# Kernel tuning notes

Measured on AMD Instinct MI355X. Metric: run time of the kernel, lower is better.

## Reference

```python
import jax, jax.numpy as jnp
import numpy as np

B, C, H, W = 8, 256, 64, 64
CR = C // 8  # reduced channels for query/key


def setup_inputs() -> dict:
    key = jax.random.key(0)
    ks = jax.random.split(key, 10)
    s = 0.02
    return {
        "x": jax.random.normal(ks[0], (B, C, H, W), dtype=jnp.float32),
        "cross_modal_features": jax.random.normal(ks[1], (B, C, H, W), dtype=jnp.float32),
        "wq": jax.random.normal(ks[2], (CR, C), dtype=jnp.float32) * s,
        "bq": jnp.zeros((CR,), dtype=jnp.float32),
        "wk": jax.random.normal(ks[3], (CR, C), dtype=jnp.float32) * s,
        "bk": jnp.zeros((CR,), dtype=jnp.float32),
        "wv": jax.random.normal(ks[4], (C, C), dtype=jnp.float32) * s,
        "bv": jnp.zeros((C,), dtype=jnp.float32),
        "wo": jax.random.normal(ks[5], (C, C), dtype=jnp.float32) * s,
        "bo": jnp.zeros((C,), dtype=jnp.float32),
        "gamma": jnp.zeros((1,), dtype=jnp.float32),
    }


def _conv1x1(w, b, t):
    # t: (B, Cin, HW) -> (B, Cout, HW); 1x1 conv == channel matmul
    return jnp.einsum("oc,bcn->bon", w, t) + b[None, :, None]


def reference(x, cross_modal_features, wq, bq, wk, bk, wv, bv, wo, bo, gamma):
    b, c, h, w = x.shape
    n = h * w
    xf = x.reshape(b, c, n)
    ff = cross_modal_features.reshape(b, c, n)
    q = _conv1x1(wq, bq, xf)          # (B, CR, N)
    k = _conv1x1(wk, bk, ff)          # (B, CR, N)
    v = _conv1x1(wv, bv, ff)          # (B, C, N)
    # attention[b,i,j] = softmax_j(q[b,:,i] . k[b,:,j])
    scores = jnp.einsum("bdi,bdj->bij", q, k)
    attn = jax.nn.softmax(scores, axis=-1)
    # out[b,c,i] = sum_j v[b,c,j] * attn[b,i,j]
    out = jnp.einsum("bcj,bij->bci", v, attn)
    out = _conv1x1(wo, bo, out).reshape(b, c, h, w)
    return gamma[0] * out + x
```

## Files before the change

### kernel.cpp

```cpp
#include <hip/hip_runtime.h>
#include <hip/hip_bf16.h>
#include <math.h>

#define B_  8
#define C_  256
#define CR_ 32
#define N_  4096

typedef __attribute__((ext_vector_type(8)))  short bf16x8;
typedef __attribute__((ext_vector_type(16))) float f32x16;
typedef __attribute__((ext_vector_type(4)))  int   int4v;

__device__ inline unsigned short f2b(float x) {
    __hip_bfloat16 h = __float2bfloat16(x);
    return __builtin_bit_cast(unsigned short, h);
}

#define GLL16(gsrc, ldst) \
    __builtin_amdgcn_global_load_lds((const __attribute__((address_space(1))) void*)(gsrc), \
                                     (__attribute__((address_space(3))) void*)(ldst), 16, 0, 0)

__global__ void pack_kernel(
    const float* __restrict__ wq, const float* __restrict__ bq,
    const float* __restrict__ wk, const float* __restrict__ bk,
    const float* __restrict__ wv, const float* __restrict__ bv,
    const float* __restrict__ wo,
    unsigned short* __restrict__ W1, unsigned short* __restrict__ W2,
    float* __restrict__ Bs1)
{
    const int r = blockIdx.x, t = threadIdx.x;
    const float L2E = 1.44269504088896340736f;
    if (r < 320) {
        float w;
        if (r < 32)      w = wq[r * C_ + t] * L2E;
        else if (r < 64) w = wk[(r - 32) * C_ + t];
        else             w = wv[(r - 64) * C_ + t];
        W1[r * C_ + t] = f2b(w);
        if (t == 0)
            Bs1[r] = (r < 32) ? bq[r] * L2E : ((r < 64) ? bk[r - 32] : bv[r - 64]);
    } else {
        W2[(r - 320) * C_ + t] = f2b(wo[(r - 320) * C_ + t]);
    }
}

__global__ __launch_bounds__(256) void convT_kernel(
    const float* __restrict__ x, const float* __restrict__ f,
    unsigned short* __restrict__ xT, unsigned short* __restrict__ fT)
{
    __shared__ float tile[64][65];
    const int t  = threadIdx.x;
    const int n0 = blockIdx.x * 64;
    const int c0 = blockIdx.y * 64;
    const int z  = blockIdx.z;
    const int b  = z >> 1;
    const float* src = (z & 1) ? f : x;
    unsigned short* dst = (z & 1) ? fT : xT;
    const size_t so = (size_t)b * C_ * N_;

    #pragma unroll
    for (int it = 0; it < 4; ++it) {
        const int cl = it * 16 + (t >> 4);
        *(float4*)&tile[cl][(t & 15) * 4] =
            *(const float4*)&src[so + (size_t)(c0 + cl) * N_ + n0 + (t & 15) * 4];
    }
    __syncthreads();

    const int nl = t >> 2;
    const int cg = (t & 3) * 16;
    unsigned short* drow = dst + ((size_t)b * N_ + n0 + nl) * C_ + c0 + cg;
    int4v w0, w1;
    #pragma unroll
    for (int e = 0; e < 4; ++e)
        w0[e] = (int)(((unsigned)f2b(tile[cg + 2*e][nl])) |
                      (((unsigned)f2b(tile[cg + 2*e + 1][nl])) << 16));
    #pragma unroll
    for (int e = 0; e < 4; ++e)
        w1[e] = (int)(((unsigned)f2b(tile[cg + 8 + 2*e][nl])) |
                      (((unsigned)f2b(tile[cg + 9 + 2*e][nl])) << 16));
    *(int4v*)(drow)     = w0;
    *(int4v*)(drow + 8) = w1;
}

__device__ __forceinline__ void gemm_mainloop(
    const unsigned short* __restrict__ Asrc,
    const unsigned short* __restrict__ Bsrc,
    unsigned short (*Ab)[32 * 32], unsigned short (*Bb)[256 * 32],
    int w, int l, f32x16& acc0, f32x16& acc1)
{
    const int jl = l & 31, hi = l >> 5;
    const int fj = (jl >> 1) & 3;

#define STAGE(KK, BUF) { \
    _Pragma("unroll") \
    for (int p = 0; p < 4; ++p) { \
        const int idx = p * 256 + w * 64 + l; \
        const int row = idx >> 2, slot = idx & 3; \
        GLL16(Bsrc + (size_t)row * 256 + (KK) * 32 + (slot ^ ((row >> 1) & 3)) * 8, \
              Bb[BUF] + (size_t)(p * 256 + w * 64) * 8); \
    } \
    if (w == 0) { \
        _Pragma("unroll") \
        for (int qq = 0; qq < 2; ++qq) { \
            const int idx = qq * 64 + l; \
            const int row = idx >> 2, slot = idx & 3; \
            GLL16(Asrc + (size_t)row * 256 + (KK) * 32 + (slot ^ ((row >> 1) & 3)) * 8, \
                  Ab[BUF] + (size_t)(qq * 64) * 8); \
        } \
    } }

    STAGE(0, 0)
    __syncthreads();

    for (int kk = 0; kk < 8; ++kk) {
        const int cur = kk & 1;
        if (kk < 7) STAGE(kk + 1, cur ^ 1)

        const unsigned short* Ac = Ab[cur];
        const unsigned short* Bc = Bb[cur];
        const bf16x8 af0 = *(const bf16x8*)&Ac[jl * 32 + ((hi ^ fj) * 8)];
        const bf16x8 af1 = *(const bf16x8*)&Ac[jl * 32 + (((2 + hi) ^ fj) * 8)];
        const int r0 = w * 64 + jl, r1 = w * 64 + 32 + jl;
        const bf16x8 bf00 = *(const bf16x8*)&Bc[r0 * 32 + ((hi ^ fj) * 8)];
        const bf16x8 bf01 = *(const bf16x8*)&Bc[r0 * 32 + (((2 + hi) ^ fj) * 8)];
        const bf16x8 bf10 = *(const bf16x8*)&Bc[r1 * 32 + ((hi ^ fj) * 8)];
        const bf16x8 bf11 = *(const bf16x8*)&Bc[r1 * 32 + (((2 + hi) ^ fj) * 8)];

        acc0 = __builtin_amdgcn_mfma_f32_32x32x16_bf16(af0, bf00, acc0, 0, 0, 0);
        acc0 = __builtin_amdgcn_mfma_f32_32x32x16_bf16(af1, bf01, acc0, 0, 0, 0);
        acc1 = __builtin_amdgcn_mfma_f32_32x32x16_bf16(af0, bf10, acc1, 0, 0, 0);
        acc1 = __builtin_amdgcn_mfma_f32_32x32x16_bf16(af1, bf11, acc1, 0, 0, 0);
        __syncthreads();
    }
#undef STAGE
}

__global__ __launch_bounds__(256) void qkv_gemm(
    const unsigned short* __restrict__ xT, const unsigned short* __restrict__ fT,
    const unsigned short* __restrict__ W1, const float* __restrict__ Bs1,
    unsigned short* __restrict__ qT, unsigned short* __restrict__ kT,
    unsigned short* __restrict__ v)
{
    __shared__ __align__(16) unsigned short Ab[2][32 * 32];
    __shared__ __align__(16) unsigned short Bb[2][256 * 32];

    const int t = threadIdx.x;
    const int w = t >> 6, l = t & 63;
    const int jl = l & 31, hi = l >> 5;
    const int bid = blockIdx.x;
    const int b  = bid & 7;
    const int r_ = bid >> 3;
    const int mt = r_ % 10;
    const int nt = r_ / 10;

    const unsigned short* Asrc = W1 + (size_t)mt * 32 * C_;
    const unsigned short* Bsrc = ((mt == 0) ? xT : fT) + (size_t)b * N_ * C_
                               + (size_t)nt * 256 * C_;

    f32x16 acc0 = (f32x16)0.f, acc1 = (f32x16)0.f;
    gemm_mainloop(Asrc, Bsrc, Ab, Bb, w, l, acc0, acc1);

    const int m0 = mt * 32;
    const int nb = nt * 256 + w * 64;
    if (mt <= 1) {
        unsigned short* dst = ((mt == 0) ? qT : kT) + (size_t)b * N_ * CR_;
        #pragma unroll
        for (int ns = 0; ns < 2; ++ns) {
            const f32x16& A = ns ? acc1 : acc0;
            const int n = nb + ns * 32 + jl;
            #pragma unroll
            for (int r4 = 0; r4 < 4; ++r4) {
                const float4 bi = *(const float4*)&Bs1[m0 + r4 * 8 + 4 * hi];
                const unsigned int d0 = (unsigned)f2b(A[r4*4+0] + bi.x) |
                                        ((unsigned)f2b(A[r4*4+1] + bi.y) << 16);
                const unsigned int d1 = (unsigned)f2b(A[r4*4+2] + bi.z) |
                                        ((unsigned)f2b(A[r4*4+3] + bi.w) << 16);
                *(uint2*)(dst + (size_t)n * CR_ + r4 * 8 + 4 * hi) = make_uint2(d0, d1);
            }
        }
    } else {
        unsigned short* dst = v + (size_t)b * C_ * N_;
        #pragma unroll
        for (int ns = 0; ns < 2; ++ns) {
            const f32x16& A = ns ? acc1 : acc0;
            const int n = nb + ns * 32 + jl;
            #pragma unroll
            for (int r4 = 0; r4 < 4; ++r4) {
                const float4 bi = *(const float4*)&Bs1[m0 + r4 * 8 + 4 * hi];
                #pragma unroll
                for (int e = 0; e < 4; ++e) {
                    const int c = m0 - 64 + e + 8 * r4 + 4 * hi;
                    dst[(size_t)c * N_ + n] = f2b(A[r4*4+e] + ((const float*)&bi)[e]);
                }
            }
        }
    }
}

__device__ inline void softmax_tile(const f32x16& s, float& lsum,
                                    bf16x8& pf0, bf16x8& pf1)
{
    float ps = 0.f;
    int wd[8];
    #pragma unroll
    for (int r = 0; r < 16; r += 2) {
        float e0 = __builtin_amdgcn_exp2f(s[r]);
        float e1 = __builtin_amdgcn_exp2f(s[r + 1]);
        ps += e0 + e1;
        int pk;
        asm("v_cvt_pk_bf16_f32 %0, %1, %2" : "=v"(pk) : "v"(e0), "v"(e1));
        wd[r >> 1] = pk;
    }
    lsum += ps;
    asm volatile("v_permlane32_swap_b32 %0, %1" : "+v"(wd[0]), "+v"(wd[2]));
    asm volatile("v_permlane32_swap_b32 %0, %1" : "+v"(wd[1]), "+v"(wd[3]));
    asm volatile("v_permlane32_swap_b32 %0, %1" : "+v"(wd[4]), "+v"(wd[6]));
    asm volatile("v_permlane32_swap_b32 %0, %1" : "+v"(wd[5]), "+v"(wd[7]));
    union { int4v i4; bf16x8 h8; } u0, u1;
    u0.i4 = (int4v){ wd[0], wd[1], wd[2], wd[3] };
    u1.i4 = (int4v){ wd[4], wd[5], wd[6], wd[7] };
    pf0 = u0.h8; pf1 = u1.h8;
}

__global__ __launch_bounds__(512) void attn_kernel(
    const unsigned short* __restrict__ qT, const unsigned short* __restrict__ kT,
    const unsigned short* __restrict__ v, unsigned short* __restrict__ aoT)
{
    __shared__ __align__(16) unsigned short Vt[2][256 * 64];
    __shared__ float lsx[2][512];

    const int t  = threadIdx.x;
    const int w  = t >> 6;
    const int l  = t & 63;
    const int jl = l & 31;
    const int hi = l >> 5;
    const int js = w & 1;
    const int ig = (w >> 1) & 1;
    const int cs = w >> 2;

    const int bid = blockIdx.x;
    const int b   = bid & 7;
    const int it  = bid >> 3;
    const int i0  = it * 128 + ig * 64;

    const unsigned short* qTb = qT + (size_t)b * N_ * CR_;
    const unsigned short* kTb = kT + (size_t)b * N_ * CR_;
    const unsigned short* vb  = v  + (size_t)b * C_ * N_;

    const bf16x8 q00 = *(const bf16x8*)(qTb + (size_t)(i0 + jl) * CR_ + hi * 8);
    const bf16x8 q01 = *(const bf16x8*)(qTb + (size_t)(i0 + jl) * CR_ + 16 + hi * 8);
    const bf16x8 q10 = *(const bf16x8*)(qTb + (size_t)(i0 + 32 + jl) * CR_ + hi * 8);
    const bf16x8 q11 = *(const bf16x8*)(qTb + (size_t)(i0 + 32 + jl) * CR_ + 16 + hi * 8);

    const unsigned short* kln = kTb + (size_t)(js * 32 + jl) * CR_ + hi * 8;

    const unsigned short* vsrc[4];
    int vdst[4];
    #pragma unroll
    for (int p = 0; p < 4; ++p) {
        const int idx = p * 512 + t;
        const int row = idx >> 3, slot = idx & 7;
        vsrc[p] = vb + (size_t)row * N_ + (slot ^ (row & 7)) * 8;
        vdst[p] = idx * 8;
    }

    f32x16 a00 = (f32x16)0.f, a01 = (f32x16)0.f, a02 = (f32x16)0.f, a03 = (f32x16)0.f;
    f32x16 a10 = (f32x16)0.f, a11 = (f32x16)0.f, a12 = (f32x16)0.f, a13 = (f32x16)0.f;
    float ls0 = 0.f, ls1 = 0.f;

    #pragma unroll
    for (int p = 0; p < 4; ++p) GLL16(vsrc[p], &Vt[0][vdst[p]]);
    bf16x8 kc0 = *(const bf16x8*)(kln);
    bf16x8 kc1 = *(const bf16x8*)(kln + 16);
    __syncthreads();

    int voff0[4], voff1[4];
    #pragma unroll
    for (int ct = 0; ct < 4; ++ct) {
        const int rv = cs * 128 + ct * 32 + jl;
        voff0[ct] = rv * 64 + (((js * 4 + hi)     ^ (rv & 7)) * 8);
        voff1[ct] = rv * 64 + (((js * 4 + 2 + hi) ^ (rv & 7)) * 8);
    }

    for (int jt = 0; jt < N_ / 64; ++jt) {
        const int cur = jt & 1;
        bf16x8 kn0 = kc0, kn1 = kc1;
        if (jt + 1 < N_ / 64) {
            const size_t jn = (size_t)(jt + 1) * 64;
            #pragma unroll
            for (int p = 0; p < 4; ++p) GLL16(vsrc[p] + jn, &Vt[cur ^ 1][vdst[p]]);
            kn0 = *(const bf16x8*)(kln + jn * CR_);
            kn1 = *(const bf16x8*)(kln + jn * CR_ + 16);
        }

        __builtin_amdgcn_s_setprio(1);
        f32x16 s0 = (f32x16)0.f, s1 = (f32x16)0.f;
        s0 = __builtin_amdgcn_mfma_f32_32x32x16_bf16(kc0, q00, s0, 0, 0, 0);
        s0 = __builtin_amdgcn_mfma_f32_32x32x16_bf16(kc1, q01, s0, 0, 0, 0);
        s1 = __builtin_amdgcn_mfma_f32_32x32x16_bf16(kc0, q10, s1, 0, 0, 0);
        s1 = __builtin_amdgcn_mfma_f32_32x32x16_bf16(kc1, q11, s1, 0, 0, 0);
        __builtin_amdgcn_s_setprio(0);

        bf16x8 p00, p01, p10, p11;
        softmax_tile(s0, ls0, p00, p01);
        softmax_tile(s1, ls1, p10, p11);

        __builtin_amdgcn_s_setprio(1);
#define PVSTEP(CT, AA, AB) { \
        const bf16x8 v0_ = *(const bf16x8*)&Vt[cur][voff0[CT]]; \
        const bf16x8 v1_ = *(const bf16x8*)&Vt[cur][voff1[CT]]; \
        AA = __builtin_amdgcn_mfma_f32_32x32x16_bf16(v0_, p00, AA, 0, 0, 0); \
        AA = __builtin_amdgcn_mfma_f32_32x32x16_bf16(v1_, p01, AA, 0, 0, 0); \
        AB = __builtin_amdgcn_mfma_f32_32x32x16_bf16(v0_, p10, AB, 0, 0, 0); \
        AB = __builtin_amdgcn_mfma_f32_32x32x16_bf16(v1_, p11, AB, 0, 0, 0); }
        PVSTEP(0, a00, a10)
        PVSTEP(1, a01, a11)
        PVSTEP(2, a02, a12)
        PVSTEP(3, a03, a13)
#undef PVSTEP
        __builtin_amdgcn_s_setprio(0);

        __syncthreads();
        kc0 = kn0; kc1 = kn1;
    }

    ls0 += __shfl_xor(ls0, 32);
    ls1 += __shfl_xor(ls1, 32);

    lsx[0][w * 64 + l] = ls0;
    lsx[1][w * 64 + l] = ls1;
    float* As = (float*)&Vt[0][0];
    const int base = (w >> 1) * 4096;

#define STORE_ACC(A, CT) { _Pragma("unroll") \
    for (int r = 0; r < 16; ++r) As[base + (CT) * 1024 + r * 64 + l] = A[r]; }
#define ADD_ACC(A, CT) { _Pragma("unroll") \
    for (int r = 0; r < 16; ++r) A[r] += As[base + (CT) * 1024 + r * 64 + l]; }

    __syncthreads();
    if (js == 1) { STORE_ACC(a00, 0) STORE_ACC(a01, 1) STORE_ACC(a02, 2) STORE_ACC(a03, 3) }
    __syncthreads();
    if (js == 0) { ADD_ACC(a00, 0) ADD_ACC(a01, 1) ADD_ACC(a02, 2) ADD_ACC(a03, 3) }
    __syncthreads();
    if (js == 1) { STORE_ACC(a10, 0) STORE_ACC(a11, 1) STORE_ACC(a12, 2) STORE_ACC(a13, 3) }
    __syncthreads();
    if (js == 0) {
        ADD_ACC(a10, 0) ADD_ACC(a11, 1) ADD_ACC(a12, 2) ADD_ACC(a13, 3)

        const float ra = 1.f / (ls0 + lsx[0][(w + 1) * 64 + l]);
        const float rb = 1.f / (ls1 + lsx[1][(w + 1) * 64 + l]);
        unsigned short* aoTb = aoT + (size_t)b * N_ * C_;
        const int ica = i0 + jl, icb = i0 + 32 + jl;
#define EPI(ACC, CT, COL, RL) { _Pragma("unroll") \
    for (int r4 = 0; r4 < 4; ++r4) { \
        const unsigned int d0 = (unsigned)f2b(ACC[r4*4+0] * (RL)) | \
                                ((unsigned)f2b(ACC[r4*4+1] * (RL)) << 16); \
        const unsigned int d1 = (unsigned)f2b(ACC[r4*4+2] * (RL)) | \
                                ((unsigned)f2b(ACC[r4*4+3] * (RL)) << 16); \
        *(uint2*)(aoTb + (size_t)(COL) * C_ + cs * 128 + (CT) * 32 + r4 * 8 + 4 * hi) \
            = make_uint2(d0, d1); } }
        EPI(a00, 0, ica, ra)
        EPI(a01, 1, ica, ra)
        EPI(a02, 2, ica, ra)
        EPI(a03, 3, ica, ra)
        EPI(a10, 0, icb, rb)
        EPI(a11, 1, icb, rb)
        EPI(a12, 2, icb, rb)
        EPI(a13, 3, icb, rb)
#undef EPI
    }
#undef STORE_ACC
#undef ADD_ACC
}

__global__ __launch_bounds__(256) void out_gemm(
    const unsigned short* __restrict__ aoT, const unsigned short* __restrict__ W2,
    const float* __restrict__ bo, const float* __restrict__ gamma,
    const float* __restrict__ x, float* __restrict__ out)
{
    __shared__ __align__(16) unsigned short Ab[2][32 * 32];
    __shared__ __align__(16) unsigned short Bb[2][256 * 32];

    const int t = threadIdx.x;
    const int w = t >> 6, l = t & 63;
    const int jl = l & 31, hi = l >> 5;
    const int bid = blockIdx.x;
    const int b  = bid & 7;
    const int r_ = bid >> 3;
    const int mt = r_ & 7;
    const int nt = r_ >> 3;

    const unsigned short* Asrc = W2 + (size_t)mt * 32 * C_;
    const unsigned short* Bsrc = aoT + (size_t)b * N_ * C_ + (size_t)nt * 256 * C_;

    f32x16 acc0 = (f32x16)0.f, acc1 = (f32x16)0.f;
    gemm_mainloop(Asrc, Bsrc, Ab, Bb, w, l, acc0, acc1);

    const float gm = gamma[0];
    const int m0 = mt * 32;
    const int nb = nt * 256 + w * 64;
    #pragma unroll
    for (int ns = 0; ns < 2; ++ns) {
        const f32x16& A = ns ? acc1 : acc0;
        const int n = nb + ns * 32 + jl;
        #pragma unroll
        for (int r4 = 0; r4 < 4; ++r4) {
            const float4 bi = *(const float4*)&bo[m0 + r4 * 8 + 4 * hi];
            #pragma unroll
            for (int e = 0; e < 4; ++e) {
                const int c = m0 + e + 8 * r4 + 4 * hi;
                const size_t o = ((size_t)b * C_ + c) * N_ + n;
                out[o] = fmaf(gm, A[r4*4+e] + ((const float*)&bi)[e], x[o]);
            }
        }
    }
}

extern "C" void kernel_launch(void* const* d_in, const int* in_sizes, int n_in,
                              void* d_out, int out_size, void* d_ws, size_t ws_size,
                              hipStream_t stream)
{
    const float* x     = (const float*)d_in[0];
    const float* f     = (const float*)d_in[1];
    const float* wq    = (const float*)d_in[2];
    const float* bq    = (const float*)d_in[3];
    const float* wk    = (const float*)d_in[4];
    const float* bk    = (const float*)d_in[5];
    const float* wv    = (const float*)d_in[6];
    const float* bv    = (const float*)d_in[7];
    const float* wo    = (const float*)d_in[8];
    const float* bo    = (const float*)d_in[9];
    const float* gamma = (const float*)d_in[10];
    float* out = (float*)d_out;

    float* Bs1 = (float*)d_ws;
    unsigned short* W1 = (unsigned short*)(Bs1 + 320);
    unsigned short* W2 = W1 + 320 * C_;
    unsigned short* xT = W2 + 256 * C_;
    unsigned short* fT = xT + (size_t)B_ * N_ * C_;
    unsigned short* qT = fT + (size_t)B_ * N_ * C_;
    unsigned short* kT = qT + (size_t)B_ * N_ * CR_;
    unsigned short* vv = kT + (size_t)B_ * N_ * CR_;
    unsigned short* aoT = vv + (size_t)B_ * C_ * N_;

    pack_kernel<<<dim3(576), 256, 0, stream>>>(wq, bq, wk, bk, wv, bv, wo, W1, W2, Bs1);
    convT_kernel<<<dim3(64, 4, 16), 256, 0, stream>>>(x, f, xT, fT);
    qkv_gemm<<<dim3(1280), 256, 0, stream>>>(xT, fT, W1, Bs1, qT, kT, vv);
    attn_kernel<<<dim3(256), 512, 0, stream>>>(qT, kT, vv, aoT);
    out_gemm<<<dim3(1024), 256, 0, stream>>>(aoT, W2, bo, gamma, x, out);
}
```

Measured before the change: 159.6 us.

## Fuse output projection GEMM and residual epilogue into attention kernel

Removes the separate out_gemm launch and the global aoT intermediate. The attention kernel now writes its normalized bf16 output tile (128 positions x 256 channels) into shared memory with an XOR swizzle. Each of its 8 waves then runs the W2 projection with MFMA against that tile and applies bias, gamma and the residual add directly. This saves a global write and read of the attention output plus one kernel launch. The cost is extra work and register pressure at the end of the attention kernel, which runs only 256 blocks, and every block reloads W2 from global memory.

```diff
diff --git a/kernel.cpp b/kernel.cpp
--- a/kernel.cpp
+++ b/kernel.cpp
@@ -223,7 +223,9 @@
 
 __global__ __launch_bounds__(512) void attn_kernel(
     const unsigned short* __restrict__ qT, const unsigned short* __restrict__ kT,
-    const unsigned short* __restrict__ v, unsigned short* __restrict__ aoT)
+    const unsigned short* __restrict__ v, const unsigned short* __restrict__ W2,
+    const float* __restrict__ bo, const float* __restrict__ gamma,
+    const float* __restrict__ x, float* __restrict__ out)
 {
     __shared__ __align__(16) unsigned short Vt[2][256 * 64];
     __shared__ float lsx[2][512];
@@ -343,73 +345,66 @@
     __syncthreads();
     if (js == 1) { STORE_ACC(a10, 0) STORE_ACC(a11, 1) STORE_ACC(a12, 2) STORE_ACC(a13, 3) }
     __syncthreads();
+    if (js == 0) { ADD_ACC(a10, 0) ADD_ACC(a11, 1) ADD_ACC(a12, 2) ADD_ACC(a13, 3) }
+    __syncthreads();
+#undef STORE_ACC
+#undef ADD_ACC
+
+    unsigned short* aoL = (unsigned short*)&Vt[0][0];
     if (js == 0) {
-        ADD_ACC(a10, 0) ADD_ACC(a11, 1) ADD_ACC(a12, 2) ADD_ACC(a13, 3)
-
         const float ra = 1.f / (ls0 + lsx[0][(w + 1) * 64 + l]);
         const float rb = 1.f / (ls1 + lsx[1][(w + 1) * 64 + l]);
-        unsigned short* aoTb = aoT + (size_t)b * N_ * C_;
-        const int ica = i0 + jl, icb = i0 + 32 + jl;
-#define EPI(ACC, CT, COL, RL) { _Pragma("unroll") \
+        const int na  = ig * 64 + jl;
+        const int nb2 = ig * 64 + 32 + jl;
+#define EPIL(ACC, CT, NL, RL) { _Pragma("unroll") \
     for (int r4 = 0; r4 < 4; ++r4) { \
         const unsigned int d0 = (unsigned)f2b(ACC[r4*4+0] * (RL)) | \
                                 ((unsigned)f2b(ACC[r4*4+1] * (RL)) << 16); \
         const unsigned int d1 = (unsigned)f2b(ACC[r4*4+2] * (RL)) | \
                                 ((unsigned)f2b(ACC[r4*4+3] * (RL)) << 16); \
-        *(uint2*)(aoTb + (size_t)(COL) * C_ + cs * 128 + (CT) * 32 + r4 * 8 + 4 * hi) \
+        const int q = cs * 16 + (CT) * 4 + r4; \
+        *(uint2*)(aoL + (NL) * 256 + ((q ^ ((NL) & 7)) * 8) + 4 * hi) \
             = make_uint2(d0, d1); } }
-        EPI(a00, 0, ica, ra)
-        EPI(a01, 1, ica, ra)
-        EPI(a02, 2, ica, ra)
-        EPI(a03, 3, ica, ra)
-        EPI(a10, 0, icb, rb)
-        EPI(a11, 1, icb, rb)
-        EPI(a12, 2, icb, rb)
-        EPI(a13, 3, icb, rb)
-#undef EPI
-    }
-#undef STORE_ACC
-#undef ADD_ACC
-}
-
-__global__ __launch_bounds__(256) void out_gemm(
-    const unsigned short* __restrict__ aoT, const unsigned short* __restrict__ W2,
-    const float* __restrict__ bo, const float* __restrict__ gamma,
-    const float* __restrict__ x, float* __restrict__ out)
-{
-    __shared__ __align__(16) unsigned short Ab[2][32 * 32];
-    __shared__ __align__(16) unsigned short Bb[2][256 * 32];
-
-    const int t = threadIdx.x;
-    const int w = t >> 6, l = t & 63;
-    const int jl = l & 31, hi = l >> 5;
-    const int bid = blockIdx.x;
-    const int b  = bid & 7;
-    const int r_ = bid >> 3;
-    const int mt = r_ & 7;
-    const int nt = r_ >> 3;
-
-    const unsigned short* Asrc = W2 + (size_t)mt * 32 * C_;
-    const unsigned short* Bsrc = aoT + (size_t)b * N_ * C_ + (size_t)nt * 256 * C_;
-
-    f32x16 acc0 = (f32x16)0.f, acc1 = (f32x16)0.f;
-    gemm_mainloop(Asrc, Bsrc, Ab, Bb, w, l, acc0, acc1);
-
-    const float gm = gamma[0];
-    const int m0 = mt * 32;
-    const int nb = nt * 256 + w * 64;
-    #pragma unroll
-    for (int ns = 0; ns < 2; ++ns) {
-        const f32x16& A = ns ? acc1 : acc0;
-        const int n = nb + ns * 32 + jl;
+        EPIL(a00, 0, na, ra)
+        EPIL(a01, 1, na, ra)
+        EPIL(a02, 2, na, ra)
+        EPIL(a03, 3, na, ra)
+        EPIL(a10, 0, nb2, rb)
+        EPIL(a11, 1, nb2, rb)
+        EPIL(a12, 2, nb2, rb)
+        EPIL(a13, 3, nb2, rb)
+#undef EPIL
+    }
+    __syncthreads();
+
+    {
+        const unsigned short* wrow = W2 + (size_t)(w * 32 + jl) * C_ + hi * 8;
+        bf16x8 af[16];
         #pragma unroll
-        for (int r4 = 0; r4 < 4; ++r4) {
-            const float4 bi = *(const float4*)&bo[m0 + r4 * 8 + 4 * hi];
+        for (int kk = 0; kk < 16; ++kk)
+            af[kk] = *(const bf16x8*)(wrow + kk * 16);
+
+        const float gm = gamma[0];
+        #pragma unroll
+        for (int nt = 0; nt < 4; ++nt) {
+            f32x16 ac = (f32x16)0.f;
             #pragma unroll
-            for (int e = 0; e < 4; ++e) {
-                const int c = m0 + e + 8 * r4 + 4 * hi;
-                const size_t o = ((size_t)b * C_ + c) * N_ + n;
-                out[o] = fmaf(gm, A[r4*4+e] + ((const float*)&bi)[e], x[o]);
+            for (int kk = 0; kk < 16; ++kk) {
+                const int q = kk * 2 + hi;
+                const bf16x8 bf = *(const bf16x8*)
+                    &aoL[(nt * 32 + jl) * 256 + ((q ^ (jl & 7)) * 8)];
+                ac = __builtin_amdgcn_mfma_f32_32x32x16_bf16(af[kk], bf, ac, 0, 0, 0);
+            }
+            const int n = it * 128 + nt * 32 + jl;
+            #pragma unroll
+            for (int r4 = 0; r4 < 4; ++r4) {
+                const float4 bi = *(const float4*)&bo[w * 32 + r4 * 8 + 4 * hi];
+                #pragma unroll
+                for (int e = 0; e < 4; ++e) {
+                    const int crow = w * 32 + e + 8 * r4 + 4 * hi;
+                    const size_t o = ((size_t)b * C_ + crow) * N_ + n;
+                    out[o] = fmaf(gm, ac[r4*4+e] + ((const float*)&bi)[e], x[o]);
+                }
             }
         }
     }
@@ -440,11 +435,9 @@
     unsigned short* qT = fT + (size_t)B_ * N_ * C_;
     unsigned short* kT = qT + (size_t)B_ * N_ * CR_;
     unsigned short* vv = kT + (size_t)B_ * N_ * CR_;
-    unsigned short* aoT = vv + (size_t)B_ * C_ * N_;
 
     pack_kernel<<<dim3(576), 256, 0, stream>>>(wq, bq, wk, bk, wv, bv, wo, W1, W2, Bs1);
     convT_kernel<<<dim3(64, 4, 16), 256, 0, stream>>>(x, f, xT, fT);
     qkv_gemm<<<dim3(1280), 256, 0, stream>>>(xT, fT, W1, Bs1, qT, kT, vv);
-    attn_kernel<<<dim3(256), 512, 0, stream>>>(qT, kT, vv, aoT);
-    out_gemm<<<dim3(1024), 256, 0, stream>>>(aoT, W2, bo, gamma, x, out);
-}
+    attn_kernel<<<dim3(256), 512, 0, stream>>>(qT, kT, vv, W2, bo, gamma, x, out);
+}
```

After: 144.7 us, median of 2. 1.1x faster.
